# Kernel tuning notes

Measured on AMD Instinct MI355X. Metric: run time of the kernel, lower is better.

The kernel has to match this reference:

```python
import jax, jax.numpy as jnp
import numpy as np

B, T, D, N = 4, 1024, 1024, 16


def setup_inputs() -> dict:
    key = jax.random.key(0)
    ks = jax.random.split(key, 16)
    s = 1.0 / np.sqrt(D)
    inp = {
        "u": jax.random.normal(ks[0], (B, T, D), jnp.float32),
        "Win": jax.random.normal(ks[1], (D, D), jnp.float32) * s,
        "b_in": jnp.zeros((D,), jnp.float32),
        "Wg": jax.random.normal(ks[2], (D, D), jnp.float32) * s,
        "bg": jnp.zeros((D,), jnp.float32),
        "Wout": jax.random.normal(ks[3], (D, D), jnp.float32) * s,
        "bout": jnp.zeros((D,), jnp.float32),
        "convw": jax.random.normal(ks[4], (D, 3), jnp.float32) * 0.5,  # depthwise k=3
        "convb": jnp.zeros((D,), jnp.float32),
        "A": -jnp.exp(jax.random.normal(ks[5], (D, N), jnp.float32) * 0.5),  # negative diag
        "Wb": jax.random.normal(ks[6], (D, N), jnp.float32) * s,
        "bb": jnp.zeros((N,), jnp.float32),
        "Wc": jax.random.normal(ks[7], (D, N), jnp.float32) * s,
        "bc": jnp.zeros((N,), jnp.float32),
        "Wdt": jax.random.normal(ks[8], (D, D), jnp.float32) * s,
        "bdt": jnp.full((D,), -2.0, jnp.float32),  # small initial dt after softplus
    }
    return inp


def _depthwise_conv3_same(x, w, b):
    # x: [B,T,D], w: [D,3], b: [D]; Conv1d(k=3, padding=1, groups=D)
    xp = jnp.pad(x, ((0, 0), (1, 1), (0, 0)))
    return xp[:, :-2] * w[:, 0] + xp[:, 1:-1] * w[:, 1] + xp[:, 2:] * w[:, 2] + b


def _selective_scan(x, A, Wb, bb, Wc, bc, Wdt, bdt):
    # x: [B,T,D]
    dt = jax.nn.softplus(x @ Wdt + bdt)            # [B,T,D]
    Bm = x @ Wb + bb                               # [B,T,N]
    Cm = x @ Wc + bc                               # [B,T,N]
    dA = jnp.exp(dt[..., None] * A)                # [B,T,D,N]
    dBx = dt[..., None] * Bm[:, :, None, :] * x[..., None]  # [B,T,D,N]

    def step(h, ins):
        dA_t, dBx_t, C_t = ins                     # [B,D,N],[B,D,N],[B,N]
        h = dA_t * h + dBx_t
        y = jnp.einsum('bdn,bn->bd', h, C_t)
        return h, y

    h0 = jnp.zeros((x.shape[0], x.shape[2], A.shape[1]), x.dtype)
    _, ys = jax.lax.scan(
        step, h0,
        (dA.transpose(1, 0, 2, 3), dBx.transpose(1, 0, 2, 3), Cm.transpose(1, 0, 2)))
    return ys.transpose(1, 0, 2)                   # [B,T,D]


def reference(u, Win, b_in, Wg, bg, Wout, bout, convw, convb, A, Wb, bb, Wc, bc, Wdt, bdt):
    x = u @ Win + b_in                             # in_proj
    x = _depthwise_conv3_same(x, convw, convb)     # depthwise conv, same padding
    x = jax.nn.silu(x)
    x_ssm = _selective_scan(x, A, Wb, bb, Wc, bc, Wdt, bdt)
    z = jax.nn.silu(u @ Wg + bg)                   # gate
    return (x_ssm * z) @ Wout + bout
```

## Files before the change

### kernel.cpp

```cpp
#include <hip/hip_runtime.h>
#include <hip/hip_bf16.h>
#include <math.h>

#define BB 4
#define TT 1024
#define DD 1024
#define NNs 16
#define MM (BB*TT)
#define MMDD ((size_t)MM*DD)
#define CHUNK 64
#define NCHUNK (TT/CHUNK)

typedef short bf16x8 __attribute__((ext_vector_type(8)));
typedef float f32x4  __attribute__((ext_vector_type(4)));

__device__ __forceinline__ float silu_f(float v)     { return v / (1.f + __expf(-v)); }
__device__ __forceinline__ float softplus_f(float v) { return fmaxf(v, 0.f) + log1pf(__expf(-fabsf(v))); }

__device__ __forceinline__ unsigned short f2bf(float f) {
  unsigned u = __builtin_bit_cast(unsigned, f);
  u += 0x7fffu + ((u >> 16) & 1u);
  return (unsigned short)(u >> 16);
}
__device__ __forceinline__ unsigned pk2(float a, float b) {
  return (unsigned)f2bf(a) | ((unsigned)f2bf(b) << 16);
}
__device__ __forceinline__ float bf2f(short s) {
  return __builtin_bit_cast(float, ((unsigned)(unsigned short)s) << 16);
}

__device__ __forceinline__ void gload16(const void* g, void* l) {
  __builtin_amdgcn_global_load_lds(
      (const __attribute__((address_space(1))) unsigned*)g,
      (__attribute__((address_space(3))) unsigned*)l, 16, 0, 0);
}

__device__ __forceinline__ int2 xcd_swz(int gx) {
  int nwg  = gx * (int)gridDim.y;
  int orig = (int)blockIdx.y * gx + (int)blockIdx.x;
  int q = nwg >> 3, r = nwg & 7;
  int xcd = orig & 7, i = orig >> 3;
  int wg = (xcd < r ? xcd * (q + 1) : r * (q + 1) + (xcd - r) * q) + i;
  return make_int2(wg % gx, wg / gx);
}

__global__ __launch_bounds__(256) void wconv_t4(
    const float* __restrict__ W0, const float* __restrict__ W1,
    const float* __restrict__ W2, const float* __restrict__ W3,
    short* __restrict__ o0, short* __restrict__ o1,
    short* __restrict__ o2, short* __restrict__ o3)
{
  const float* W; short* Wt;
  switch (blockIdx.z) {
    case 0:  W = W0; Wt = o0; break;
    case 1:  W = W1; Wt = o1; break;
    case 2:  W = W2; Wt = o2; break;
    default: W = W3; Wt = o3; break;
  }
  __shared__ float t[32][33];
  int n0 = blockIdx.x * 32, k0 = blockIdx.y * 32;
  int r  = threadIdx.x >> 3;
  int c4 = (threadIdx.x & 7) * 4;
  float4 v = *(const float4*)(W + (size_t)(k0 + r) * DD + n0 + c4);
  t[r][c4+0] = v.x; t[r][c4+1] = v.y; t[r][c4+2] = v.z; t[r][c4+3] = v.w;
  __syncthreads();
  short q0 = (short)f2bf(t[c4+0][r]);
  short q1 = (short)f2bf(t[c4+1][r]);
  short q2 = (short)f2bf(t[c4+2][r]);
  short q3 = (short)f2bf(t[c4+3][r]);
  *(short4*)(Wt + (size_t)(n0 + r) * DD + k0 + c4) = make_short4(q0, q1, q2, q3);
}

__global__ __launch_bounds__(256) void wbc_t(
    const float* __restrict__ Wb, const float* __restrict__ Wc,
    short* __restrict__ Wbct)
{
  int idx = blockIdx.x * 256 + threadIdx.x;
  int k = idx & (DD - 1);
  int n = idx >> 10;
  const float* W = (n < 16) ? Wb : Wc;
  Wbct[(size_t)n * DD + k] = (short)f2bf(W[(size_t)k * NNs + (n & 15)]);
}

__global__ __launch_bounds__(256) void to_bf16(
    const float* __restrict__ in, short* __restrict__ out)
{
  size_t i = (size_t)(blockIdx.x * 256 + threadIdx.x) * 8;
  float4 a = *(const float4*)(in + i);
  float4 b = *(const float4*)(in + i + 4);
  *(uint4*)(out + i) = make_uint4(pk2(a.x,a.y), pk2(a.z,a.w),
                                  pk2(b.x,b.y), pk2(b.z,b.w));
}

__device__ __forceinline__ void gemm_core(
    const short* __restrict__ Ab, const short* __restrict__ Bt,
    const float* __restrict__ bias, float* __restrict__ C,
    int Nn, int K, int kBase, int kLen, int bm0, int bn0, int epi,
    short* As, short* Bs)
{
  const int tid  = threadIdx.x;
  const int lane = tid & 63;
  const int w    = tid >> 6;
  const int wm0  = (w >> 1) * 64;
  const int wn0  = (w & 1) * 64;

  const int srow = tid >> 3;
  const int scol = ((tid & 7) ^ ((tid >> 3) & 7)) << 3;

  const short* gA = Ab + (size_t)(bm0 + srow) * K + kBase + scol;
  const short* gB = Bt + (size_t)(bn0 + srow) * K + kBase + scol;
  char* ldsA = (char*)As;
  char* ldsB = (char*)Bs;
  const int wuni = w * 1024;

  f32x4 acc[4][4];
  const f32x4 zz = {0.f, 0.f, 0.f, 0.f};
  #pragma unroll
  for (int m = 0; m < 4; m++)
    #pragma unroll
    for (int n = 0; n < 4; n++) acc[m][n] = zz;

  const int fr  = lane & 15;
  const int ks  = (lane >> 4) << 3;
  const int swz = (fr & 7) << 3;

  const int NT = kLen >> 6;

  #pragma unroll
  for (int i = 0; i < 4; i++) {
    gload16(gA + (size_t)(i * 32) * K, ldsA + i * 4096 + wuni);
    gload16(gB + (size_t)(i * 32) * K, ldsB + i * 4096 + wuni);
  }
  __syncthreads();

  for (int t = 0; t < NT; ++t) {
    const int cur = t & 1;
    if (t + 1 < NT) {
      const int k1 = (t + 1) << 6;
      const int bo = (cur ^ 1) * 16384;
      #pragma unroll
      for (int i = 0; i < 4; i++) {
        gload16(gA + (size_t)(i * 32) * K + k1, ldsA + bo + i * 4096 + wuni);
        gload16(gB + (size_t)(i * 32) * K + k1, ldsB + bo + i * 4096 + wuni);
      }
    }
    const short* Ac = As + cur * 8192;
    const short* Bc = Bs + cur * 8192;
    #pragma unroll
    for (int s = 0; s < 2; s++) {
      const int cs = ((s << 5) | ks) ^ swz;
      bf16x8 af[4], bf[4];
      #pragma unroll
      for (int m = 0; m < 4; m++)
        af[m] = *(const bf16x8*)&Ac[(wm0 + m*16 + fr) * 64 + cs];
      #pragma unroll
      for (int n = 0; n < 4; n++)
        bf[n] = *(const bf16x8*)&Bc[(wn0 + n*16 + fr) * 64 + cs];
      #pragma unroll
      for (int m = 0; m < 4; m++)
        #pragma unroll
        for (int n = 0; n < 4; n++)
          acc[m][n] = __builtin_amdgcn_mfma_f32_16x16x32_bf16(af[m], bf[n], acc[m][n], 0, 0, 0);
    }
    __syncthreads();
  }

  const int orow = (lane >> 4) * 4;
  const int ocol = lane & 15;
  #pragma unroll
  for (int n = 0; n < 4; n++) {
    const int col = bn0 + wn0 + n*16 + ocol;
    const float bv = bias ? bias[col] : 0.f;
    #pragma unroll
    for (int m = 0; m < 4; m++) {
      #pragma unroll
      for (int r = 0; r < 4; r++) {
        float v = acc[m][n][r] + bv;
        if (epi == 1) v = silu_f(v);
        else if (epi == 2) v = softplus_f(v);
        C[(size_t)(bm0 + wm0 + m*16 + orow + r) * Nn + col] = v;
      }
    }
  }
}

__global__ __launch_bounds__(256) void gemm_ing_k(
    const short* __restrict__ ub,
    const short* __restrict__ Wti, const short* __restrict__ Wtg,
    const float* __restrict__ b_in, const float* __restrict__ bg,
    float* __restrict__ x1, float* __restrict__ z)
{
  __shared__ short As[2*128*64];
  __shared__ short Bs[2*128*64];
  int2 p = xcd_swz(gridDim.x);
  const int gate = p.x >> 3;
  gemm_core(ub, gate ? Wtg : Wti, gate ? bg : b_in, gate ? z : x1,
            DD, DD, 0, DD, p.y * 128, (p.x & 7) * 128, gate ? 1 : 0, As, Bs);
}

__global__ __launch_bounds__(256) void gemm_out_k(
    const short* __restrict__ xsb, const short* __restrict__ Wto,
    float* __restrict__ O0, float* __restrict__ O1)
{
  __shared__ short As[2*128*64];
  __shared__ short Bs[2*128*64];
  int2 p = xcd_swz(gridDim.x);
  const int s = blockIdx.z;
  gemm_core(xsb, Wto, nullptr, s ? O1 : O0,
            DD, DD, s * 512, 512, p.y * 128, p.x * 128, 0, As, Bs);
}

__global__ __launch_bounds__(256) void gemm_dtbc_k(
    const short* __restrict__ xb, const short* __restrict__ Wtd,
    const short* __restrict__ Wbct,
    float* __restrict__ d0, float* __restrict__ d1,
    float* __restrict__ B0, float* __restrict__ B1,
    float* __restrict__ C0, float* __restrict__ C1)
{
  __shared__ short As[2*128*64];
  __shared__ short Bs[2*128*64];
  __shared__ short Cs[2*32*64];
  int2 p = xcd_swz(gridDim.x);
  const int sp  = blockIdx.z;
  const int kB  = sp * 512;
  const int bx  = p.x;
  const int bm0 = p.y * 128;
  const int bn0 = bx * 128;
  float* dOut = sp ? d1 : d0;
  float* bOut = sp ? B1 : B0;
  float* cOut = sp ? C1 : C0;

  const int tid  = threadIdx.x;
  const int lane = tid & 63;
  const int w    = tid >> 6;
  const int wm0  = (w >> 1) * 64;
  const int wn0  = (w & 1) * 64;

  const int srow = tid >> 3;
  const int scol = ((tid & 7) ^ ((tid >> 3) & 7)) << 3;

  const short* gA = xb   + (size_t)(bm0 + srow) * DD + kB + scol;
  const short* gB = Wtd  + (size_t)(bn0 + srow) * DD + kB + scol;
  const short* gC = Wbct + (size_t)srow * DD + kB + scol;
  char* ldsA = (char*)As;
  char* ldsB = (char*)Bs;
  char* ldsC = (char*)Cs;
  const int wuni = w * 1024;

  f32x4 acc[4][4];
  const f32x4 zz = {0.f, 0.f, 0.f, 0.f};
  #pragma unroll
  for (int m = 0; m < 4; m++)
    #pragma unroll
    for (int n = 0; n < 4; n++) acc[m][n] = zz;
  f32x4 accbc = zz;

  const int fr  = lane & 15;
  const int ks  = (lane >> 4) << 3;
  const int swz = (fr & 7) << 3;

  #pragma unroll
  for (int i = 0; i < 4; i++) {
    gload16(gA + (size_t)(i * 32) * DD, ldsA + i * 4096 + wuni);
    gload16(gB + (size_t)(i * 32) * DD, ldsB + i * 4096 + wuni);
  }
  gload16(gC, ldsC + wuni);
  __syncthreads();

  for (int t = 0; t < 8; ++t) {
    const int cur = t & 1;
    if (t + 1 < 8) {
      const int k1 = (t + 1) << 6;
      const int bo = (cur ^ 1) * 16384;
      #pragma unroll
      for (int i = 0; i < 4; i++) {
        gload16(gA + (size_t)(i * 32) * DD + k1, ldsA + bo + i * 4096 + wuni);
        gload16(gB + (size_t)(i * 32) * DD + k1, ldsB + bo + i * 4096 + wuni);
      }
      gload16(gC + k1, ldsC + (cur ^ 1) * 4096 + wuni);
    }
    const short* Ac = As + cur * 8192;
    const short* Bc = Bs + cur * 8192;
    const short* Cc = Cs + cur * 2048;
    #pragma unroll
    for (int s = 0; s < 2; s++) {
      const int cs = ((s << 5) | ks) ^ swz;
      bf16x8 af[4], bf[4];
      #pragma unroll
      for (int m = 0; m < 4; m++)
        af[m] = *(const bf16x8*)&Ac[(wm0 + m*16 + fr) * 64 + cs];
      #pragma unroll
      for (int n = 0; n < 4; n++)
        bf[n] = *(const bf16x8*)&Bc[(wn0 + n*16 + fr) * 64 + cs];
      #pragma unroll
      for (int m = 0; m < 4; m++)
        #pragma unroll
        for (int n = 0; n < 4; n++)
          acc[m][n] = __builtin_amdgcn_mfma_f32_16x16x32_bf16(af[m], bf[n], acc[m][n], 0, 0, 0);
      if (w < 2) {
        bf16x8 abc = *(const bf16x8*)&Ac[(bx*16 + fr) * 64 + cs];
        bf16x8 bbc = *(const bf16x8*)&Cc[((w << 4) + fr) * 64 + cs];
        accbc = __builtin_amdgcn_mfma_f32_16x16x32_bf16(abc, bbc, accbc, 0, 0, 0);
      }
    }
    __syncthreads();
  }

  const int orow = (lane >> 4) * 4;
  const int ocol = lane & 15;
  #pragma unroll
  for (int n = 0; n < 4; n++) {
    const int col = bn0 + wn0 + n*16 + ocol;
    #pragma unroll
    for (int m = 0; m < 4; m++) {
      #pragma unroll
      for (int r = 0; r < 4; r++)
        dOut[(size_t)(bm0 + wm0 + m*16 + orow + r) * DD + col] = acc[m][n][r];
    }
  }
  if (w < 2) {
    float* dst = (w == 0) ? bOut : cOut;
    #pragma unroll
    for (int r = 0; r < 4; r++) {
      int row = bm0 + bx*16 + orow + r;
      dst[(size_t)row * NNs + ocol] = accbc[r];
    }
  }
}

__global__ __launch_bounds__(256) void conv_silu(
    const float* __restrict__ x1, const float* __restrict__ cw,
    const float* __restrict__ cb, short* __restrict__ xb)
{
  int idx = blockIdx.x * 256 + threadIdx.x;
  int d4 = idx & (DD/4 - 1);
  int bt = idx >> 8;
  int t  = bt & (TT - 1);
  const float4* b4 = (const float4*)x1;
  size_t ri = (size_t)bt * (DD/4) + d4;
  float4 zz = make_float4(0.f, 0.f, 0.f, 0.f);
  float4 vc = b4[ri];
  float4 vm = (t > 0)      ? b4[ri - DD/4] : zz;
  float4 vp = (t < TT - 1) ? b4[ri + DD/4] : zz;
  float rm[4] = {vm.x, vm.y, vm.z, vm.w};
  float rc[4] = {vc.x, vc.y, vc.z, vc.w};
  float rp[4] = {vp.x, vp.y, vp.z, vp.w};
  float o[4];
  #pragma unroll
  for (int j = 0; j < 4; j++) {
    int d = d4*4 + j;
    float v = rm[j]*cw[d*3+0] + rc[j]*cw[d*3+1] + rp[j]*cw[d*3+2] + cb[d];
    o[j] = silu_f(v);
  }
  ((uint2*)xb)[ri] = make_uint2(pk2(o[0], o[1]), pk2(o[2], o[3]));
}

__global__ __launch_bounds__(256) void scan_local(
    const float* __restrict__ d0, const float* __restrict__ d1,
    const float* __restrict__ bdt, const short* __restrict__ xb,
    const float* __restrict__ B0, const float* __restrict__ B1,
    const float* __restrict__ bb, const float* __restrict__ A,
    float* __restrict__ P, float* __restrict__ S)
{
  __shared__ float Bsh[CHUNK*NNs];
  int bid = blockIdx.x;
  int dblk = bid & 3;
  int c = (bid >> 2) & 15;
  int b = bid >> 6;
  int d = dblk*256 + threadIdx.x;
  int t0 = c * CHUNK;
  size_t bo = (size_t)(b*TT + t0)*NNs;
  for (int i = threadIdx.x; i < CHUNK*NNs; i += 256)
    Bsh[i] = B0[bo + i] + B1[bo + i] + bb[i & 15];
  float a[NNs];
  #pragma unroll
  for (int n = 0; n < NNs; n++) a[n] = A[d*NNs + n];
  const float bdtv = bdt[d];
  __syncthreads();
  float h[NNs], p[NNs];
  #pragma unroll
  for (int n = 0; n < NNs; n++) { h[n] = 0.f; p[n] = 1.f; }
  size_t base = (size_t)(b*TT + t0)*DD + d;
  for (int tt = 0; tt < CHUNK; tt++) {
    size_t gi = base + (size_t)tt*DD;
    float dtv = softplus_f(d0[gi] + d1[gi] + bdtv);
    float xv  = bf2f(xb[gi]);
    float dx = dtv * xv;
    #pragma unroll
    for (int n = 0; n < NNs; n++) {
      float e = __expf(dtv * a[n]);
      h[n] = fmaf(e, h[n], dx * Bsh[tt*NNs + n]);
      p[n] *= e;
    }
  }
  size_t o = ((size_t)((b*NCHUNK + c)*DD + d)) * NNs;
  #pragma unroll
  for (int n = 0; n < NNs; n += 4) {
    *(float4*)&P[o+n] = make_float4(p[n], p[n+1], p[n+2], p[n+3]);
    *(float4*)&S[o+n] = make_float4(h[n], h[n+1], h[n+2], h[n+3]);
  }
}

__global__ __launch_bounds__(256) void scan_combine(
    const float* __restrict__ P, const float* __restrict__ S,
    float* __restrict__ H0)
{
  int g = blockIdx.x*256 + threadIdx.x;
  int n = g & 15; int d = (g >> 4) & 1023; int b = g >> 14;
  float h = 0.f;
  for (int c = 0; c < NCHUNK; c++) {
    size_t idx = ((size_t)((b*NCHUNK + c)*DD + d)) * NNs + n;
    float pv = P[idx], sv = S[idx];
    H0[idx] = h;
    h = fmaf(pv, h, sv);
  }
}

__global__ __launch_bounds__(256) void scan_y(
    const float* __restrict__ d0, const float* __restrict__ d1,
    const float* __restrict__ bdt, const short* __restrict__ xb,
    const float* __restrict__ B0, const float* __restrict__ B1,
    const float* __restrict__ bb,
    const float* __restrict__ C0, const float* __restrict__ C1,
    const float* __restrict__ bc,
    const float* __restrict__ A,  const float* __restrict__ H0,
    const float* __restrict__ z,  short* __restrict__ xsb)
{
  __shared__ float Bsh[CHUNK*NNs];
  __shared__ float Csh[CHUNK*NNs];
  int bid = blockIdx.x;
  int dblk = bid & 3;
  int c = (bid >> 2) & 15;
  int b = bid >> 6;
  int d = dblk*256 + threadIdx.x;
  int t0 = c * CHUNK;
  size_t bo = (size_t)(b*TT + t0)*NNs;
  for (int i = threadIdx.x; i < CHUNK*NNs; i += 256) {
    Bsh[i] = B0[bo + i] + B1[bo + i] + bb[i & 15];
    Csh[i] = C0[bo + i] + C1[bo + i] + bc[i & 15];
  }
  float a[NNs];
  #pragma unroll
  for (int n = 0; n < NNs; n++) a[n] = A[d*NNs + n];
  const float bdtv = bdt[d];
  size_t ho = ((size_t)((b*NCHUNK + c)*DD + d)) * NNs;
  float h[NNs];
  #pragma unroll
  for (int n = 0; n < NNs; n += 4) {
    float4 h4 = *(const float4*)&H0[ho+n];
    h[n] = h4.x; h[n+1] = h4.y; h[n+2] = h4.z; h[n+3] = h4.w;
  }
  __syncthreads();
  size_t base = (size_t)(b*TT + t0)*DD + d;
  for (int tt = 0; tt < CHUNK; tt++) {
    size_t gi = base + (size_t)tt*DD;
    float dtv = softplus_f(d0[gi] + d1[gi] + bdtv);
    float xv  = bf2f(xb[gi]);
    float dx = dtv * xv;
    float y = 0.f;
    #pragma unroll
    for (int n = 0; n < NNs; n++) {
      float e = __expf(dtv * a[n]);
      h[n] = fmaf(e, h[n], dx * Bsh[tt*NNs + n]);
      y = fmaf(h[n], Csh[tt*NNs + n], y);
    }
    xsb[gi] = (short)f2bf(y * z[gi]);
  }
}

__global__ __launch_bounds__(256) void out_epi(
    const float* __restrict__ O0, const float* __restrict__ O1,
    const float* __restrict__ bout, float* __restrict__ out)
{
  size_t i = (size_t)(blockIdx.x * 256 + threadIdx.x) * 4;
  int col = (int)(i & (DD - 1));
  float4 a = *(const float4*)(O0 + i);
  float4 b = *(const float4*)(O1 + i);
  float4 bv = *(const float4*)(bout + col);
  *(float4*)(out + i) = make_float4(a.x + b.x + bv.x, a.y + b.y + bv.y,
                                    a.z + b.z + bv.z, a.w + b.w + bv.w);
}

extern "C" void kernel_launch(void* const* d_in, const int* in_sizes, int n_in,
                              void* d_out, int out_size, void* d_ws, size_t ws_size,
                              hipStream_t stream)
{
  const float* u     = (const float*)d_in[0];
  const float* Win   = (const float*)d_in[1];
  const float* b_in  = (const float*)d_in[2];
  const float* Wg    = (const float*)d_in[3];
  const float* bg    = (const float*)d_in[4];
  const float* Wout  = (const float*)d_in[5];
  const float* bout  = (const float*)d_in[6];
  const float* convw = (const float*)d_in[7];
  const float* convb = (const float*)d_in[8];
  const float* A     = (const float*)d_in[9];
  const float* Wb    = (const float*)d_in[10];
  const float* bb    = (const float*)d_in[11];
  const float* Wc    = (const float*)d_in[12];
  const float* bc    = (const float*)d_in[13];
  const float* Wdt   = (const float*)d_in[14];
  const float* bdt   = (const float*)d_in[15];
  float* out = (float*)d_out;

  float* ws = (float*)d_ws;
  float* x1 = ws;
  float* z  = x1 + MMDD;
  float* d0 = z  + MMDD;
  float* d1 = d0 + MMDD;
  float* B0 = d1 + MMDD;
  float* B1 = B0 + (size_t)MM*NNs;
  float* C0 = B1 + (size_t)MM*NNs;
  float* C1 = C0 + (size_t)MM*NNs;
  short* ub  = (short*)(C1 + (size_t)MM*NNs);
  short* xb  = ub  + MMDD;
  short* Wti = xb  + MMDD;
  short* Wtg = Wti + (size_t)DD*DD;
  short* Wtd = Wtg + (size_t)DD*DD;
  short* Wto = Wtd + (size_t)DD*DD;
  short* Wbct = Wto + (size_t)DD*DD;
  float* P  = x1;
  float* S  = P + (size_t)BB*NCHUNK*DD*NNs;
  float* H0 = P;
  float* O0 = d0;
  float* O1 = d1;
  short* xsb = ub;

  wconv_t4<<<dim3(DD/32, DD/32, 4), 256, 0, stream>>>(
      Win, Wg, Wdt, Wout, Wti, Wtg, Wtd, Wto);
  wbc_t<<<(32*DD)/256, 256, 0, stream>>>(Wb, Wc, Wbct);
  to_bf16<<<(MMDD/8)/256, 256, 0, stream>>>(u, ub);

  gemm_ing_k<<<dim3(16, MM/128), 256, 0, stream>>>(ub, Wti, Wtg, b_in, bg, x1, z);
  conv_silu<<<(MMDD/4)/256, 256, 0, stream>>>(x1, convw, convb, xb);
  gemm_dtbc_k<<<dim3(8, MM/128, 2), 256, 0, stream>>>(
      xb, Wtd, Wbct, d0, d1, B0, B1, C0, C1);
  scan_local  <<<BB*NCHUNK*(DD/256), 256, 0, stream>>>(
      d0, d1, bdt, xb, B0, B1, bb, A, P, S);
  scan_combine<<<(BB*DD*NNs)/256, 256, 0, stream>>>(P, S, H0);
  scan_y      <<<BB*NCHUNK*(DD/256), 256, 0, stream>>>(
      d0, d1, bdt, xb, B0, B1, bb, C0, C1, bc, A, H0, z, xsb);
  gemm_out_k<<<dim3(8, MM/128, 2), 256, 0, stream>>>(xsb, Wto, O0, O1);
  out_epi<<<(MMDD/4)/256, 256, 0, stream>>>(O0, O1, bout, out);
}
```

Measured before the change: 297.4 us.

## Halve scan chunk size, prefetch next-step loads, cache softplus dt between scan passes

Halves the scan chunk length to CHUNK 32, which doubles the number of blocks in scan_local and scan_y and gives the GPU more parallelism. Both scan loops now software-prefetch the next timestep's operands into registers. scan_local writes the computed softplus dt back over d0, so scan_y reads a single precomputed dt instead of d0+d1 and repeating the softplus. In exchange, the chunk-combine pass has twice as many sequential steps and the P/S buffers double in size. The d0 buffer is also overwritten, which only works because nothing later reads it before gemm_out reuses it.

```diff
diff --git a/kernel.cpp b/kernel.cpp
--- a/kernel.cpp
+++ b/kernel.cpp
@@ -8,7 +8,7 @@
 #define NNs 16
 #define MM (BB*TT)
 #define MMDD ((size_t)MM*DD)
-#define CHUNK 64
+#define CHUNK 32
 #define NCHUNK (TT/CHUNK)
 
 typedef short bf16x8 __attribute__((ext_vector_type(8)));
@@ -356,7 +356,7 @@
 }
 
 __global__ __launch_bounds__(256) void scan_local(
-    const float* __restrict__ d0, const float* __restrict__ d1,
+    float* __restrict__ d0, const float* __restrict__ d1,
     const float* __restrict__ bdt, const short* __restrict__ xb,
     const float* __restrict__ B0, const float* __restrict__ B1,
     const float* __restrict__ bb, const float* __restrict__ A,
@@ -365,8 +365,8 @@
   __shared__ float Bsh[CHUNK*NNs];
   int bid = blockIdx.x;
   int dblk = bid & 3;
-  int c = (bid >> 2) & 15;
-  int b = bid >> 6;
+  int c = (bid >> 2) & (NCHUNK - 1);
+  int b = bid >> 7;
   int d = dblk*256 + threadIdx.x;
   int t0 = c * CHUNK;
   size_t bo = (size_t)(b*TT + t0)*NNs;
@@ -381,11 +381,17 @@
   #pragma unroll
   for (int n = 0; n < NNs; n++) { h[n] = 0.f; p[n] = 1.f; }
   size_t base = (size_t)(b*TT + t0)*DD + d;
+  float pd0 = d0[base], pd1 = d1[base];
+  short pxb = xb[base];
   for (int tt = 0; tt < CHUNK; tt++) {
-    size_t gi = base + (size_t)tt*DD;
-    float dtv = softplus_f(d0[gi] + d1[gi] + bdtv);
-    float xv  = bf2f(xb[gi]);
-    float dx = dtv * xv;
+    float cd0 = pd0, cd1 = pd1; short cxb = pxb;
+    if (tt + 1 < CHUNK) {
+      size_t gn = base + (size_t)(tt + 1)*DD;
+      pd0 = d0[gn]; pd1 = d1[gn]; pxb = xb[gn];
+    }
+    float dtv = softplus_f(cd0 + cd1 + bdtv);
+    d0[base + (size_t)tt*DD] = dtv;
+    float dx = dtv * bf2f(cxb);
     #pragma unroll
     for (int n = 0; n < NNs; n++) {
       float e = __expf(dtv * a[n]);
@@ -417,8 +423,7 @@
 }
 
 __global__ __launch_bounds__(256) void scan_y(
-    const float* __restrict__ d0, const float* __restrict__ d1,
-    const float* __restrict__ bdt, const short* __restrict__ xb,
+    const float* __restrict__ dtf, const short* __restrict__ xb,
     const float* __restrict__ B0, const float* __restrict__ B1,
     const float* __restrict__ bb,
     const float* __restrict__ C0, const float* __restrict__ C1,
@@ -430,8 +435,8 @@
   __shared__ float Csh[CHUNK*NNs];
   int bid = blockIdx.x;
   int dblk = bid & 3;
-  int c = (bid >> 2) & 15;
-  int b = bid >> 6;
+  int c = (bid >> 2) & (NCHUNK - 1);
+  int b = bid >> 7;
   int d = dblk*256 + threadIdx.x;
   int t0 = c * CHUNK;
   size_t bo = (size_t)(b*TT + t0)*NNs;
@@ -442,7 +447,6 @@
   float a[NNs];
   #pragma unroll
   for (int n = 0; n < NNs; n++) a[n] = A[d*NNs + n];
-  const float bdtv = bdt[d];
   size_t ho = ((size_t)((b*NCHUNK + c)*DD + d)) * NNs;
   float h[NNs];
   #pragma unroll
@@ -452,19 +456,22 @@
   }
   __syncthreads();
   size_t base = (size_t)(b*TT + t0)*DD + d;
+  float pdt = dtf[base]; short pxb = xb[base]; float pz = z[base];
   for (int tt = 0; tt < CHUNK; tt++) {
-    size_t gi = base + (size_t)tt*DD;
-    float dtv = softplus_f(d0[gi] + d1[gi] + bdtv);
-    float xv  = bf2f(xb[gi]);
-    float dx = dtv * xv;
+    float cdt = pdt; short cxb = pxb; float cz = pz;
+    if (tt + 1 < CHUNK) {
+      size_t gn = base + (size_t)(tt + 1)*DD;
+      pdt = dtf[gn]; pxb = xb[gn]; pz = z[gn];
+    }
+    float dx = cdt * bf2f(cxb);
     float y = 0.f;
     #pragma unroll
     for (int n = 0; n < NNs; n++) {
-      float e = __expf(dtv * a[n]);
+      float e = __expf(cdt * a[n]);
       h[n] = fmaf(e, h[n], dx * Bsh[tt*NNs + n]);
       y = fmaf(h[n], Csh[tt*NNs + n], y);
     }
-    xsb[gi] = (short)f2bf(y * z[gi]);
+    xsb[base + (size_t)tt*DD] = (short)f2bf(y * cz);
   }
 }
 
@@ -539,7 +546,7 @@
       d0, d1, bdt, xb, B0, B1, bb, A, P, S);
   scan_combine<<<(BB*DD*NNs)/256, 256, 0, stream>>>(P, S, H0);
   scan_y      <<<BB*NCHUNK*(DD/256), 256, 0, stream>>>(
-      d0, d1, bdt, xb, B0, B1, bb, C0, C1, bc, A, H0, z, xsb);
+      d0, xb, B0, B1, bb, C0, C1, bc, A, H0, z, xsb);
   gemm_out_k<<<dim3(8, MM/128, 2), 256, 0, stream>>>(xsb, Wto, O0, O1);
   out_epi<<<(MMDD/4)/256, 256, 0, stream>>>(O0, O1, bout, out);
 }
```

Result: faster. 249.3 us (-16.2%).
